# Kernel tuning notes

Measured on AMD Instinct MI355X. Metric: run time of the kernel, lower is better.

## Reference

```python
import jax, jax.numpy as jnp
from jax import lax
import numpy as np

# ---- static config (mirrors init_kwargs) ----
B, IN_CH, OUT_CH, IN_SIZE, OUT_SIZE, W_DIM, K = 8, 512, 512, 64, 64, 512, 3
UP, DOWN, TAPS = 2, 2, 12
IN_CUTOFF = OUT_CUTOFF = 32.0
HALF_W = 32.0 * (np.sqrt(2.0) - 1.0)
TMP_FS = 128.0
CLAMP, SLOPE, ACT_GAIN = 256.0, 0.2, float(np.sqrt(2.0))
HID = 64  # SIREN hidden dim

def _kaiser_beta(a):
    if a > 50:
        return 0.1102 * (a - 8.7)
    if a > 21:
        return 0.5842 * (a - 21.0) ** 0.4 + 0.07886 * (a - 21.0)
    return 0.0

def _firwin(numtaps, cutoff, width, fs):
    # windowed-sinc lowpass (scipy.signal.firwin with kaiser window)
    nyq = fs / 2.0
    atten = 2.285 * (numtaps - 1) * np.pi * (width / nyq) + 7.95
    beta = _kaiser_beta(atten)
    m = np.arange(numtaps) - (numtaps - 1) / 2.0
    c = cutoff / nyq
    h = c * np.sinc(c * m) * np.kaiser(numtaps, beta)
    return (h / h.sum()).astype(np.float32)

UP_FILTER = _firwin(TAPS, IN_CUTOFF, 2 * HALF_W, TMP_FS)
DOWN_FILTER = _firwin(TAPS, OUT_CUTOFF, 2 * HALF_W, TMP_FS)
_pt = (OUT_SIZE - 1) * DOWN + 1 - (IN_SIZE + K - 1) * UP + 2 * TAPS - 2
PAD_LO = (_pt + UP) // 2
PAD_HI = _pt - PAD_LO  # (9, 8)

# ---- SynthesisKernel statics: init_size=3, density=1, down_factor=2, 4-tap filter ----
KG_OUT = 3
KG_IN = KG_OUT * 2  # 6
_kc = KG_OUT / 2.0  # out_cutoff = 1.5
KG_FILT = _firwin(4, _kc, 2 * _kc * (np.sqrt(2.0) - 1.0), _kc * 2 * 2 ** 0.1)
_knots = np.arange(KG_OUT) - KG_OUT // 2
_s2 = (KG_OUT + 2 + 1) / 12.0  # gauss_spline sigma^2 for order out_size+2
_g = np.exp(-_knots ** 2 / (2 * _s2)) / np.sqrt(2 * np.pi * _s2)
GAUSS = (np.sqrt(np.outer(_g, _g)) * 2.0).astype(np.float32)
# affine_grid (align_corners=False) coords scaled by 0.5*in_size/out_size = 1.0
_c = (((2 * np.arange(KG_IN) + 1) / KG_IN) - 1.0) * (0.5 * KG_IN / KG_OUT)
_X, _Y = np.meshgrid(_c, _c)
GRID = np.stack([_X, _Y], -1).reshape(-1, 2).astype(np.float32)  # [36, 2] (x, y)

def _dwconv(x, k):
    return lax.conv_general_dilated(x, k, (1, 1), 'VALID',
        feature_group_count=x.shape[1], dimension_numbers=('NCHW', 'OIHW', 'NCHW'))

def _upfirdn2d(x, f, up=1, down=1, padding=(0, 0, 0, 0), gain=1.0):
    b, c, h, w = x.shape
    if up > 1:
        x = jnp.pad(x[:, :, :, None, :, None], ((0, 0), (0, 0), (0, 0), (0, up - 1), (0, 0), (0, up - 1)))
        x = x.reshape(b, c, h * up, w * up)
    px0, px1, py0, py1 = padding
    x = jnp.pad(x, ((0, 0), (0, 0), (py0, py1), (px0, px1)))
    fl = jnp.flip(f)  # true convolution, like upfirdn2d reference
    x = _dwconv(x, jnp.tile(fl.reshape(1, 1, -1, 1), (c, 1, 1, 1)))
    x = _dwconv(x, jnp.tile(fl.reshape(1, 1, 1, -1), (c, 1, 1, 1)))
    if down > 1:
        x = x[:, :, ::down, ::down]
    return x * gain

def _forward(x, w, affine_w, affine_b, style_weight, bias, siren_w0, siren_b0,
             siren_w1, siren_b1, siren_w2, siren_b2, siren_w3, siren_b3,
             kscale, magnitude_ema):
    # affine: styles [B, IN_CH], weight_gain = 1/sqrt(w_dim), bias_init = 1
    styles = w @ (affine_w.T * (1.0 / np.sqrt(W_DIM))) + affine_b
    # SynthesisKernel: SIREN over 6x6 grid -> filtered/downsampled 3x3 depthwise kernel
    g = jnp.asarray(GRID)
    h1 = jnp.sin(30.0 * (g @ siren_w0 + siren_b0))
    h1 = jnp.sin(h1 @ siren_w1 + siren_b1)
    h1 = jnp.sin(h1 @ siren_w2 + siren_b2)
    kw = h1 @ siren_w3 + siren_b3                                    # [36, IN_CH]
    kw = kw * (jax.nn.sigmoid(kscale / 10.0) * 2.0)
    kw = kw.reshape(1, KG_IN, KG_IN, IN_CH).transpose(3, 0, 1, 2)    # [IN_CH,1,6,6]
    kw = _upfirdn2d(kw, jnp.asarray(KG_FILT), down=2, padding=(1, 1, 1, 1))  # [IN_CH,1,3,3]
    kw = kw - kw.mean(axis=(1, 2, 3), keepdims=True)
    kw = kw * lax.rsqrt(jnp.mean(kw * kw, axis=(1, 2, 3), keepdims=True))
    kw = kw * jnp.asarray(GAUSS)
    # depthwise conv, input_gain = magnitude_ema.rsqrt(), padding = conv_kernel - 1
    kw = kw * lax.rsqrt(magnitude_ema)
    xp = jnp.pad(x, ((0, 0), (0, 0), (K - 1, K - 1), (K - 1, K - 1)))
    x = _dwconv(xp, kw)                                              # [B,IN_CH,66,66]
    # modulated 1x1 conv with demodulation (modulated_conv2d with kh=kw=1)
    sw = style_weight[:, :, 0, 0]                                    # [O, I]
    sw = sw * lax.rsqrt(jnp.mean(sw * sw, axis=1, keepdims=True))
    sn = styles * lax.rsqrt(jnp.mean(styles * styles))
    wb = sw[None, :, :] * sn[:, None, :]                             # [B, O, I]
    wb = wb * lax.rsqrt(jnp.sum(wb * wb, axis=2, keepdims=True) + 1e-8)
    x = jnp.einsum('bihw,boi->bohw', x, wb)
    # filtered leaky relu: bias -> FIR up(2) -> lrelu*sqrt(2), clamp -> FIR down(2)
    x = x + bias[None, :, None, None]
    x = _upfirdn2d(x, jnp.asarray(UP_FILTER), up=UP,
                   padding=(PAD_LO, PAD_HI, PAD_LO, PAD_HI), gain=float(UP * UP))
    x = jnp.where(x < 0, SLOPE * x, x) * ACT_GAIN
    x = jnp.clip(x, -CLAMP, CLAMP)
    x = _upfirdn2d(x, jnp.asarray(DOWN_FILTER), down=DOWN)           # [B,O,64,64]
    return x

def setup_inputs() -> dict:
    key = jax.random.key(0)
    ks = jax.random.split(key, 10)
    ch = float(np.sqrt(6.0 / HID))  # SIREN hidden init bound
    return {
        'x': jax.random.normal(ks[0], (B, IN_CH, IN_SIZE, IN_SIZE), jnp.float32),
        'w': jax.random.normal(ks[1], (B, W_DIM), jnp.float32),
        'affine_w': jax.random.normal(ks[2], (IN_CH, W_DIM), jnp.float32),
        'affine_b': jnp.ones((IN_CH,), jnp.float32),
        'style_weight': jax.random.normal(ks[3], (OUT_CH, IN_CH, 1, 1), jnp.float32),
        'bias': jnp.zeros((OUT_CH,), jnp.float32),
        'siren_w0': jax.random.uniform(ks[4], (2, HID), jnp.float32, -0.5, 0.5),
        'siren_b0': jnp.zeros((HID,), jnp.float32),
        'siren_w1': jax.random.uniform(ks[5], (HID, HID), jnp.float32, -ch, ch),
        'siren_b1': jnp.zeros((HID,), jnp.float32),
        'siren_w2': jax.random.uniform(ks[6], (HID, HID), jnp.float32, -ch, ch),
        'siren_b2': jnp.zeros((HID,), jnp.float32),
        'siren_w3': jax.random.uniform(ks[7], (HID, IN_CH), jnp.float32, -ch, ch),
        'siren_b3': jnp.zeros((IN_CH,), jnp.float32),
        'kscale': jax.random.normal(ks[8], (IN_CH,), jnp.float32),
        'magnitude_ema': jnp.ones((), jnp.float32),
    }

def reference(x, w, affine_w, affine_b, style_weight, bias, siren_w0, siren_b0,
              siren_w1, siren_b1, siren_w2, siren_b2, siren_w3, siren_b3,
              kscale, magnitude_ema):
    return _forward(x, w, affine_w, affine_b, style_weight, bias, siren_w0, siren_b0,
                    siren_w1, siren_b1, siren_w2, siren_b2, siren_w3, siren_b3,
                    kscale, magnitude_ema)
```

## Files before the change

kernel.cpp:

```cpp
#include <hip/hip_runtime.h>
#include <stdint.h>
#include <math.h>

typedef uint16_t u16; typedef uint32_t u32;
typedef __bf16 bf16x8 __attribute__((ext_vector_type(8)));
typedef float  f32x4  __attribute__((ext_vector_type(4)));
typedef u32 __attribute__((address_space(1))) gu32;
typedef u32 __attribute__((address_space(3))) lu32;

#define FOFF_FUP    0
#define FOFF_KG     16
#define FOFF_GAUSS  24
#define FOFF_PART   40
#define FOFF_H3     48
#define FOFF_STYLES 2368
#define FOFF_KK     6464
#define OFFB_WB  ((size_t)65536)
#define OFFB_MUV ((size_t)4456448)
#define OFFB_MUH ((size_t)4459520)
#define OFFB_MDV ((size_t)4487168)
#define OFFB_MDH ((size_t)4489216)
#define OFFB_XT  ((size_t)(8u<<20))
#define OFFB_Y1  ((size_t)(45u<<20))

static __device__ __forceinline__ u16 f2b(float f) {
  union { float f; u32 u; } v; v.f = f;
  u32 u = v.u;
  return (u16)((u + 0x7fffu + ((u >> 16) & 1u)) >> 16);
}
static __device__ __forceinline__ float b2f(u16 h) {
  union { u32 u; float f; } v; v.u = ((u32)h) << 16; return v.f;
}

static __device__ float bessel_i0f(float x) {
  float t = x * 0.5f, t2 = t * t;
  float term = 1.f, sum = 1.f;
  for (int k = 1; k < 32; k++) {
    term *= t2 / ((float)k * (float)k);
    sum += term;
    if (term < 1e-8f * sum) break;
  }
  return sum;
}
static __device__ void firwin_devf(int numtaps, float cutoff, float width, float fs, float* out) {
  float nyq = fs * 0.5f;
  float atten = 2.285f * (numtaps - 1) * 3.14159265358979f * (width / nyq) + 7.95f;
  float beta;
  if (atten > 50.f) beta = 0.1102f * (atten - 8.7f);
  else if (atten > 21.f) beta = 0.5842f * powf(atten - 21.f, 0.4f) + 0.07886f * (atten - 21.f);
  else beta = 0.f;
  float c = cutoff / nyq;
  float i0b = bessel_i0f(beta);
  float h[16]; float s = 0.f;
  for (int n = 0; n < numtaps; n++) {
    float m = n - (numtaps - 1) * 0.5f;
    float x = c * m;
    float pix = 3.14159265358979f * x;
    float snc = (x == 0.f) ? 1.f : __sinf(pix) / pix;
    float r = 2.f * n / (float)(numtaps - 1) - 1.f;
    float arg = 1.f - r * r; if (arg < 0.f) arg = 0.f;
    float kais = bessel_i0f(beta * sqrtf(arg)) / i0b;
    h[n] = c * snc * kais; s += h[n];
  }
  for (int n = 0; n < numtaps; n++) out[n] = h[n] / s;
}

__global__ void k_setup(const float* __restrict__ sw0, const float* __restrict__ sb0,
                        const float* __restrict__ sw1, const float* __restrict__ sb1,
                        const float* __restrict__ sw2, const float* __restrict__ sb2,
                        float* __restrict__ ws) {
  __shared__ float hA[2304], hB[2304];
  int t = threadIdx.x;
  if (t == 0) {
    firwin_devf(12, 32.f, 2.f * 32.f * 0.41421356237309515f, 128.f, ws + FOFF_FUP);
  }
  if (t == 64) {
    float kc = 1.5f;
    firwin_devf(4, kc, 2.f * kc * 0.41421356237309515f, kc * 2.f * 1.0717734625362931f, ws + FOFF_KG);
  }
  if (t == 128) {
    float s2 = 0.5f;
    float gk[3];
    for (int k = 0; k < 3; k++) {
      float kn = (float)(k - 1);
      gk[k] = expf(-kn * kn / (2.f * s2)) / sqrtf(2.f * 3.14159265358979f * s2);
    }
    for (int i = 0; i < 3; i++)
      for (int j = 0; j < 3; j++)
        ws[FOFF_GAUSS + i * 3 + j] = sqrtf(gk[i] * gk[j]) * 2.f;
  }
  if (t >= 192 && t < 200) ws[FOFF_PART + t - 192] = 0.f;
  for (int idx = t; idx < 2304; idx += 256) {
    int p = idx >> 6, u = idx & 63;
    float gx = (2.f * (p % 6) + 1.f) / 6.f - 1.f;
    float gy = (2.f * (p / 6) + 1.f) / 6.f - 1.f;
    hA[idx] = sinf(30.f * (gx * sw0[u] + gy * sw0[64 + u] + sb0[u]));
  }
  __syncthreads();
  {
    float fuv[12];
    #pragma unroll
    for (int i = 0; i < 12; i++) fuv[i] = ws[FOFF_FUP + i];
    char* wsb = (char*)ws;
    u16* muv = (u16*)(wsb + OFFB_MUV);
    u16* muh = (u16*)(wsb + OFFB_MUH);
    u16* mdv = (u16*)(wsb + OFFB_MDV);
    u16* mdh = (u16*)(wsb + OFFB_MDH);
    for (int i = t; i < 48 * 32; i += 256) {
      int r = i >> 5, s = i & 31;
      float v = 0.f;
      if (r < 42 && s < 26) {
        int d = (r >> 1) + 5 - s;
        if (d >= 0 && d <= 5) v = fuv[2 * d + (r & 1)];
      }
      muv[i] = f2b(v);
    }
    for (int i = t; i < 144 * 96; i += 256) {
      int n = i / 96, j = i - n * 96;
      float v = 0.f;
      if (n < 138 && j < 66) {
        int k = (n >> 1) + 1 - j;
        if (k >= 0 && k <= 5) v = fuv[2 * k + (n & 1)];
      }
      muh[i] = f2b(v);
    }
    for (int i = t; i < 16 * 64; i += 256) {
      int R = i >> 6, ar = i & 63;
      float v = 0.f;
      if (ar < 42) {
        int q = ar - 2 * R;
        if (q >= 0 && q <= 11) v = fuv[11 - q];
      }
      mdv[i] = f2b(v);
    }
    for (int i = t; i < 64 * 160; i += 256) {
      int ox = i / 160, ac = i - ox * 160;
      float v = 0.f;
      if (ac < 138) {
        int q = ac - 2 * ox;
        if (q >= 0 && q <= 11) v = fuv[11 - q];
      }
      mdh[i] = f2b(v);
    }
  }
  for (int idx = t; idx < 2304; idx += 256) {
    int p = idx >> 6, u = idx & 63;
    float acc = sb1[u];
    for (int v = 0; v < 64; v++) acc += hA[p * 64 + v] * sw1[v * 64 + u];
    hB[idx] = sinf(acc);
  }
  __syncthreads();
  for (int idx = t; idx < 2304; idx += 256) {
    int p = idx >> 6, u = idx & 63;
    float acc = sb2[u];
    for (int v = 0; v < 64; v++) acc += hB[p * 64 + v] * sw2[v * 64 + u];
    ws[FOFF_H3 + idx] = sinf(acc);
  }
}

__global__ void k_stkw(const float* __restrict__ w, const float* __restrict__ aw,
                       const float* __restrict__ ab,
                       const float* __restrict__ w3, const float* __restrict__ b3,
                       const float* __restrict__ kscale, const float* __restrict__ emap,
                       float* __restrict__ ws) {
  __shared__ __align__(16) char sm[18944];
  int t = threadIdx.x;
  if (blockIdx.x < 64) {
    float* wl  = (float*)sm;
    float* red = (float*)(sm + 2048);
    int b = blockIdx.x >> 3, j0 = (blockIdx.x & 7) * 64;
    wl[t] = w[b * 512 + t]; wl[t + 256] = w[b * 512 + 256 + t];
    __syncthreads();
    int j = j0 + (t & 63), kq = t >> 6;
    const f32x4* ar = (const f32x4*)(aw + (size_t)j * 512 + kq * 128);
    const f32x4* wv = (const f32x4*)(wl + kq * 128);
    float acc = 0.f;
    for (int k = 0; k < 32; k++) {
      f32x4 a = ar[k], c = wv[k];
      acc += a[0] * c[0] + a[1] * c[1] + a[2] * c[2] + a[3] * c[3];
    }
    red[t] = acc; __syncthreads();
    if (t < 64) {
      float sv = (red[t] + red[t + 64] + red[t + 128] + red[t + 192]) * 0.04419417382415922f + ab[j0 + t];
      ws[FOFF_STYLES + b * 512 + j0 + t] = sv;
      float p = sv * sv;
      for (int m = 32; m; m >>= 1) p += __shfl_xor(p, m);
      if (t == 0) atomicAdd(&ws[FOFF_PART + b], p);
    }
  } else {
    float* h3l = (float*)sm;
    float (*kw6)[37] = (float(*)[37])(sm + 9216);
    int c0 = (blockIdx.x - 64) * 64;
    for (int i = t; i < 2304; i += 256) h3l[i] = ws[FOFF_H3 + i];
    __syncthreads();
    int cl = t & 63, pg = t >> 6;
    int c = c0 + cl;
    float acc[9];
    #pragma unroll
    for (int q = 0; q < 9; q++) acc[q] = b3[c];
    for (int v = 0; v < 64; v++) {
      float wv = w3[v * 512 + c];
      #pragma unroll
      for (int q = 0; q < 9; q++) acc[q] += h3l[(pg * 9 + q) * 64 + v] * wv;
    }
    float sc = 2.f / (1.f + expf(-kscale[c] * 0.1f));
    #pragma unroll
    for (int q = 0; q < 9; q++) kw6[cl][pg * 9 + q] = acc[q] * sc;
    __syncthreads();
    if (t < 64) {
      float kg[4];
      #pragma unroll
      for (int i = 0; i < 4; i++) kg[i] = ws[FOFF_KG + i];
      float pre[9];
      for (int u = 0; u < 3; u++)
        for (int vv = 0; vv < 3; vv++) {
          float s = 0.f;
          for (int t1 = 0; t1 < 4; t1++) {
            int a = 2 * u + t1 - 1;
            if (a < 0 || a > 5) continue;
            for (int t2 = 0; t2 < 4; t2++) {
              int bb = 2 * vv + t2 - 1;
              if (bb < 0 || bb > 5) continue;
              s += kg[3 - t1] * kg[3 - t2] * kw6[t][a * 6 + bb];
            }
          }
          pre[u * 3 + vv] = s;
        }
      float m = 0.f;
      #pragma unroll
      for (int q = 0; q < 9; q++) m += pre[q];
      m *= (1.f / 9.f);
      float ms = 0.f;
      #pragma unroll
      for (int q = 0; q < 9; q++) { pre[q] -= m; ms += pre[q] * pre[q]; }
      ms *= (1.f / 9.f);
      float r = 1.f / sqrtf(ms);
      float re = 1.f / sqrtf(emap[0]);
      #pragma unroll
      for (int q = 0; q < 9; q++)
        ws[FOFF_KK + q * 512 + (c0 + t)] = pre[q] * r * ws[FOFF_GAUSS + q] * re;
    }
  }
}

__global__ void k_wb(const float* __restrict__ sw, const float* __restrict__ ws,
                     u16* __restrict__ wb) {
  int wv = threadIdx.x >> 6, lane = threadIdx.x & 63;
  int o = blockIdx.x * 4 + wv, b = blockIdx.y;
  float ssum = 0.f;
  #pragma unroll
  for (int i = 0; i < 8; i++) ssum += ws[FOFF_PART + i];
  float rsn = 1.f / sqrtf(ssum * (1.f / 4096.f));
  float swv[8], stv[8];
  float s2 = 0.f;
  #pragma unroll
  for (int q = 0; q < 8; q++) {
    int i = lane + q * 64;
    swv[q] = sw[(size_t)o * 512 + i];
    stv[q] = ws[FOFF_STYLES + b * 512 + i];
    s2 += swv[q] * swv[q];
  }
  for (int m = 32; m; m >>= 1) s2 += __shfl_xor(s2, m);
  float r1 = 1.f / sqrtf(s2 * (1.f / 512.f));
  float tv[8]; float t2 = 0.f;
  #pragma unroll
  for (int q = 0; q < 8; q++) { tv[q] = swv[q] * r1 * stv[q] * rsn; t2 += tv[q] * tv[q]; }
  for (int m = 32; m; m >>= 1) t2 += __shfl_xor(t2, m);
  float r2 = 1.f / sqrtf(t2 + 1e-8f);
  #pragma unroll
  for (int q = 0; q < 8; q++)
    wb[((size_t)b * 512 + o) * 512 + lane + q * 64] = f2b(tv[q] * r2);
}

__global__ void k_transpose(const float* __restrict__ x, u16* __restrict__ xT) {
  int h = blockIdx.x, c0 = blockIdx.y * 64, b = blockIdx.z;
  int t = threadIdx.x;
  __shared__ u16 tl[64][66];
  int wcol = t & 63, cbase = t >> 6;
  const float* xp = x + ((size_t)(b * 512 + c0)) * 4096 + h * 64;
  #pragma unroll
  for (int k = 0; k < 16; k++) {
    int ci = cbase + k * 4;
    tl[ci][wcol] = f2b(xp[(size_t)ci * 4096 + wcol]);
  }
  __syncthreads();
  int cp = t & 31, wbse = t >> 5;
  u32* dst = (u32*)(xT + ((size_t)b * 4096 + h * 64) * 512 + c0);
  #pragma unroll
  for (int k = 0; k < 8; k++) {
    int w_ = wbse + k * 8;
    u32 v0 = tl[cp * 2][w_], v1 = tl[cp * 2 + 1][w_];
    dst[w_ * 256 + cp] = v0 | (v1 << 16);
  }
}

__global__ void k_dw(const u16* __restrict__ xT, const float* __restrict__ ws,
                     u16* __restrict__ y1) {
  int tile = blockIdx.x, b = blockIdx.y, t = threadIdx.x;
  int c2 = t * 2;
  float2 kk[9];
  #pragma unroll
  for (int q = 0; q < 9; q++) kk[q] = *(const float2*)&ws[FOFF_KK + q * 512 + c2];
  #pragma unroll 2
  for (int pos = 0; pos < 16; pos++) {
    int hw = tile * 16 + pos;
    if (hw < 4356) {
      int h = hw / 66, w_ = hw - h * 66;
      float a0 = 0.f, a1 = 0.f;
      for (int i = 0; i < 3; i++) {
        int ih = h - 2 + i; if (ih < 0 || ih >= 64) continue;
        for (int j = 0; j < 3; j++) {
          int iw = w_ - 2 + j; if (iw < 0 || iw >= 64) continue;
          u32 xv = *(const u32*)(xT + ((size_t)b * 4096 + ih * 64 + iw) * 512 + c2);
          float2 kv = kk[i * 3 + j];
          a0 += kv.x * b2f((u16)xv);
          a1 += kv.y * b2f((u16)(xv >> 16));
        }
      }
      ((u32*)y1)[(((size_t)b * 4480 + hw) * 512 + c2) >> 1] = (u32)f2b(a0) | ((u32)f2b(a1) << 16);
    } else {
      ((u32*)y1)[(((size_t)b * 4480 + hw) * 512 + c2) >> 1] = 0u;
    }
  }
}

__launch_bounds__(256, 4)
__global__ void k_gemm(const u16* __restrict__ wbm, const u16* __restrict__ y1,
                       const float* __restrict__ bias, u16* __restrict__ y2) {
  int lid = blockIdx.x + 35 * (blockIdx.y + (blockIdx.z << 2));
  int b  = lid & 7;
  int s_ = lid >> 3;
  int mt = s_ & 3;
  int nt = s_ >> 2;
  int t = threadIdx.x, lane = t & 63, wv = t >> 6;
  int wm = wv >> 1, wn = wv & 1;
  __shared__ u16 Al[4096];
  __shared__ u16 Bl[4096];
  f32x4 acc[4][4];
  #pragma unroll
  for (int i = 0; i < 4; i++)
    #pragma unroll
    for (int j = 0; j < 4; j++)
      acc[i][j] = (f32x4){0.f, 0.f, 0.f, 0.f};

  const size_t Abase = (size_t)b * 512 + mt * 128;
  const size_t Bbase = (size_t)b * 4480 + nt * 128;
  int lrow = lane >> 2, dch = lane & 3;
  int cp = lane >> 4;

  for (int ks = 0; ks < 16; ks++) {
    int k0 = ks * 32;
    __syncthreads();
    #pragma unroll
    for (int half = 0; half < 2; half++) {
      int rbase = half * 64 + wv * 16;
      int row = rbase + lrow;
      int gch = dch ^ ((row >> 1) & 3);
      const u16* ga = wbm + (Abase + row) * 512 + k0 + gch * 8;
      const u16* gb = y1 + (Bbase + row) * 512 + k0 + gch * 8;
      __builtin_amdgcn_global_load_lds((const gu32*)ga, (lu32*)&Al[rbase * 32], 16, 0, 0);
      __builtin_amdgcn_global_load_lds((const gu32*)gb, (lu32*)&Bl[rbase * 32], 16, 0, 0);
    }
    asm volatile("s_waitcnt vmcnt(0)" ::: "memory");
    __syncthreads();
    bf16x8 af[4], bfr[4];
    #pragma unroll
    for (int mi = 0; mi < 4; mi++) {
      int row = wm * 64 + mi * 16 + (lane & 15);
      af[mi] = *(const bf16x8*)&Al[row * 32 + ((cp ^ ((row >> 1) & 3)) * 8)];
    }
    #pragma unroll
    for (int ni = 0; ni < 4; ni++) {
      int row = wn * 64 + ni * 16 + (lane & 15);
      bfr[ni] = *(const bf16x8*)&Bl[row * 32 + ((cp ^ ((row >> 1) & 3)) * 8)];
    }
    #pragma unroll
    for (int mi = 0; mi < 4; mi++)
      #pragma unroll
      for (int ni = 0; ni < 4; ni++)
        acc[mi][ni] = __builtin_amdgcn_mfma_f32_16x16x32_bf16(af[mi], bfr[ni], acc[mi][ni], 0, 0, 0);
  }
  int col0 = nt * 128 + wn * 64 + (lane & 15);
  int rb = (lane >> 4) * 4;
  #pragma unroll
  for (int mi = 0; mi < 4; mi++) {
    #pragma unroll
    for (int j = 0; j < 4; j++) {
      int o = mt * 128 + wm * 64 + mi * 16 + rb + j;
      float bv = bias[o];
      size_t rowoff = ((size_t)b * 512 + o) * 4480;
      #pragma unroll
      for (int ni = 0; ni < 4; ni++)
        y2[rowoff + col0 + ni * 16] = f2b(acc[mi][ni][j] + bv);
    }
  }
}

__launch_bounds__(256, 5)
__global__ void k_updown(const u16* __restrict__ y2,
                         const u16* __restrict__ muv, const u16* __restrict__ muh,
                         const u16* __restrict__ mdv, const u16* __restrict__ mdh,
                         float* __restrict__ out) {
  int g = blockIdx.x, o = blockIdx.y, b = blockIdx.z;
  int t = threadIdx.x, lane = t & 63, wv = t >> 6;
  int l15 = lane & 15, cp = lane >> 4, rb = cp * 4;
  __shared__ __align__(16) char smem[30720];
  u16* Yt  = (u16*)smem;
  u16* At  = (u16*)smem;
  u16* T1u = (u16*)(smem + 20736);
  u16* T3u = (u16*)(smem + 20736);
  const int out_r0 = g * 16;
  const int yrow0 = out_r0 - 4;
  const u16* plane = y2 + ((size_t)b * 512 + o) * 4480;

  for (int i = t; i < 1920; i += 256) ((float4*)smem)[i] = make_float4(0.f, 0.f, 0.f, 0.f);
  __syncthreads();
  for (int idx = t; idx < 26 * 66; idx += 256) {
    int s = idx / 66, j = idx - 66 * s;
    int grow = yrow0 + s;
    u16 v = 0;
    if (grow >= 0 && grow < 66) v = plane[(size_t)grow * 66 + j];
    Yt[j * 40 + s] = v;
  }
  __syncthreads();

  __builtin_amdgcn_s_setprio(1);
  for (int tau = wv; tau < 15; tau += 4) {
    int mi = tau / 5, ni = tau - mi * 5;
    bf16x8 a = *(const bf16x8*)&muv[(mi * 16 + l15) * 32 + cp * 8];
    bf16x8 bfr = *(const bf16x8*)&Yt[(ni * 16 + l15) * 40 + cp * 8];
    f32x4 acc = (f32x4){0.f, 0.f, 0.f, 0.f};
    acc = __builtin_amdgcn_mfma_f32_16x16x32_bf16(a, bfr, acc, 0, 0, 0);
    #pragma unroll
    for (int j = 0; j < 4; j++)
      T1u[(mi * 16 + rb + j) * 104 + ni * 16 + l15] = f2b(acc[j]);
  }
  __builtin_amdgcn_s_setprio(0);
  __syncthreads();

  __builtin_amdgcn_s_setprio(1);
  for (int ni = wv; ni < 9; ni += 4) {
    bf16x8 bh[3];
    #pragma unroll
    for (int ks = 0; ks < 3; ks++)
      bh[ks] = *(const bf16x8*)&muh[(ni * 16 + l15) * 96 + ks * 32 + cp * 8];
    #pragma unroll
    for (int mi = 0; mi < 3; mi++) {
      f32x4 acc = (f32x4){0.f, 0.f, 0.f, 0.f};
      #pragma unroll
      for (int ks = 0; ks < 3; ks++) {
        bf16x8 a = *(const bf16x8*)&T1u[(mi * 16 + l15) * 104 + ks * 32 + cp * 8];
        acc = __builtin_amdgcn_mfma_f32_16x16x32_bf16(a, bh[ks], acc, 0, 0, 0);
      }
      int c = ni * 16 + l15;
      u16 pv[4];
      #pragma unroll
      for (int j = 0; j < 4; j++) {
        float x = acc[j];
        x = fmaxf(x, 0.2f * x) * 5.65685424949238f;
        x = fminf(fmaxf(x, -256.f), 256.f);
        pv[j] = f2b(x);
      }
      u32 lo = (u32)pv[0] | ((u32)pv[1] << 16);
      u32 hi = (u32)pv[2] | ((u32)pv[3] << 16);
      *(uint2*)&At[c * 72 + mi * 16 + rb] = make_uint2(lo, hi);
    }
  }
  __builtin_amdgcn_s_setprio(0);
  __syncthreads();

  __builtin_amdgcn_s_setprio(1);
  {
    bf16x8 a0 = *(const bf16x8*)&mdv[l15 * 64 + cp * 8];
    bf16x8 a1 = *(const bf16x8*)&mdv[l15 * 64 + 32 + cp * 8];
    for (int ni = wv; ni < 9; ni += 4) {
      f32x4 acc = (f32x4){0.f, 0.f, 0.f, 0.f};
      bf16x8 b0 = *(const bf16x8*)&At[(ni * 16 + l15) * 72 + cp * 8];
      acc = __builtin_amdgcn_mfma_f32_16x16x32_bf16(a0, b0, acc, 0, 0, 0);
      bf16x8 b1 = *(const bf16x8*)&At[(ni * 16 + l15) * 72 + 32 + cp * 8];
      acc = __builtin_amdgcn_mfma_f32_16x16x32_bf16(a1, b1, acc, 0, 0, 0);
      #pragma unroll
      for (int j = 0; j < 4; j++)
        T3u[(rb + j) * 168 + ni * 16 + l15] = f2b(acc[j]);
    }
  }
  __builtin_amdgcn_s_setprio(0);
  __syncthreads();

  {
    __builtin_amdgcn_s_setprio(1);
    f32x4 acc = (f32x4){0.f, 0.f, 0.f, 0.f};
    #pragma unroll
    for (int ks = 0; ks < 5; ks++) {
      bf16x8 a = *(const bf16x8*)&T3u[l15 * 168 + ks * 32 + cp * 8];
      bf16x8 bfr = *(const bf16x8*)&mdh[(wv * 16 + l15) * 160 + ks * 32 + cp * 8];
      acc = __builtin_amdgcn_mfma_f32_16x16x32_bf16(a, bfr, acc, 0, 0, 0);
    }
    __builtin_amdgcn_s_setprio(0);
    float* op = out + (((size_t)b * 512 + o) * 64 + out_r0) * 64;
    #pragma unroll
    for (int j = 0; j < 4; j++)
      op[(rb + j) * 64 + wv * 16 + l15] = acc[j];
  }
}

extern "C" void kernel_launch(void* const* d_in, const int* in_sizes, int n_in,
                              void* d_out, int out_size, void* d_ws, size_t ws_size,
                              hipStream_t stream) {
  const float* x     = (const float*)d_in[0];
  const float* w     = (const float*)d_in[1];
  const float* aw    = (const float*)d_in[2];
  const float* ab    = (const float*)d_in[3];
  const float* swgt  = (const float*)d_in[4];
  const float* bias  = (const float*)d_in[5];
  const float* sw0   = (const float*)d_in[6];
  const float* sb0   = (const float*)d_in[7];
  const float* sw1   = (const float*)d_in[8];
  const float* sb1   = (const float*)d_in[9];
  const float* sw2   = (const float*)d_in[10];
  const float* sb2   = (const float*)d_in[11];
  const float* sw3   = (const float*)d_in[12];
  const float* sb3   = (const float*)d_in[13];
  const float* kscl  = (const float*)d_in[14];
  const float* ema   = (const float*)d_in[15];

  float* ws  = (float*)d_ws;
  char*  wsb = (char*)d_ws;
  u16* wbp = (u16*)(wsb + OFFB_WB);
  u16* xT  = (u16*)(wsb + OFFB_XT);
  u16* y2  = xT;
  u16* y1  = (u16*)(wsb + OFFB_Y1);
  u16* muv = (u16*)(wsb + OFFB_MUV);
  u16* muh = (u16*)(wsb + OFFB_MUH);
  u16* mdv = (u16*)(wsb + OFFB_MDV);
  u16* mdh = (u16*)(wsb + OFFB_MDH);

  k_setup<<<dim3(1), dim3(256), 0, stream>>>(sw0, sb0, sw1, sb1, sw2, sb2, ws);
  k_stkw<<<dim3(72), dim3(256), 0, stream>>>(w, aw, ab, sw3, sb3, kscl, ema, ws);
  k_wb<<<dim3(128, 8), dim3(256), 0, stream>>>(swgt, ws, wbp);
  k_transpose<<<dim3(64, 8, 8), dim3(256), 0, stream>>>(x, xT);
  k_dw<<<dim3(280, 8), dim3(256), 0, stream>>>(xT, ws, y1);
  k_gemm<<<dim3(35, 4, 8), dim3(256), 0, stream>>>(wbp, y1, bias, y2);
  k_updown<<<dim3(4, 512, 8), dim3(256), 0, stream>>>(y2, muv, muh, mdv, mdh, (float*)d_out);
}
```

Measured before the change: 300.6 us.

## Fuse NCHW-to-NHWC transpose into depthwise conv using LDS row staging

Replaces the separate transpose kernel and the depthwise 3x3 kernel with one kernel. Each block stages three padded input rows for 64 channels in shared memory, converted to bf16, then computes the 66 output columns for one row straight from LDS. This removes the round trip through the intermediate bf16 NHWC buffer and one kernel launch, and reads each input value once per block instead of up to nine times from global memory. In exchange, each input row is loaded by three blocks, the fp32 global loads are strided per channel, and the LDS accesses may bank-conflict.

```diff
diff --git a/kernel.cpp b/kernel.cpp
--- a/kernel.cpp
+++ b/kernel.cpp
@@ -20,7 +20,7 @@
 #define OFFB_MUH ((size_t)4459520)
 #define OFFB_MDV ((size_t)4487168)
 #define OFFB_MDH ((size_t)4489216)
-#define OFFB_XT  ((size_t)(8u<<20))
+#define OFFB_Y2  ((size_t)(8u<<20))
 #define OFFB_Y1  ((size_t)(45u<<20))
 
 static __device__ __forceinline__ u16 f2b(float f) {
@@ -272,55 +272,58 @@
     wb[((size_t)b * 512 + o) * 512 + lane + q * 64] = f2b(tv[q] * r2);
 }
 
-__global__ void k_transpose(const float* __restrict__ x, u16* __restrict__ xT) {
-  int h = blockIdx.x, c0 = blockIdx.y * 64, b = blockIdx.z;
-  int t = threadIdx.x;
-  __shared__ u16 tl[64][66];
-  int wcol = t & 63, cbase = t >> 6;
-  const float* xp = x + ((size_t)(b * 512 + c0)) * 4096 + h * 64;
-  #pragma unroll
-  for (int k = 0; k < 16; k++) {
-    int ci = cbase + k * 4;
-    tl[ci][wcol] = f2b(xp[(size_t)ci * 4096 + wcol]);
-  }
-  __syncthreads();
-  int cp = t & 31, wbse = t >> 5;
-  u32* dst = (u32*)(xT + ((size_t)b * 4096 + h * 64) * 512 + c0);
-  #pragma unroll
-  for (int k = 0; k < 8; k++) {
-    int w_ = wbse + k * 8;
-    u32 v0 = tl[cp * 2][w_], v1 = tl[cp * 2 + 1][w_];
-    dst[w_ * 256 + cp] = v0 | (v1 << 16);
-  }
-}
-
-__global__ void k_dw(const u16* __restrict__ xT, const float* __restrict__ ws,
-                     u16* __restrict__ y1) {
-  int tile = blockIdx.x, b = blockIdx.y, t = threadIdx.x;
-  int c2 = t * 2;
+__global__ void k_tdw(const float* __restrict__ x, const float* __restrict__ ws,
+                      u16* __restrict__ y1) {
+  int h = blockIdx.x, cb = blockIdx.y, b = blockIdx.z;
+  int c0 = cb * 64, t = threadIdx.x;
+  if (h == 66) {
+    u32* dst = (u32*)y1;
+    for (int idx = t; idx < 124 * 32; idx += 256) {
+      int row = idx >> 5, col = idx & 31;
+      dst[((size_t)b * 4480 + 4356 + row) * 256 + (c0 >> 1) + col] = 0u;
+    }
+    return;
+  }
+  __shared__ u16 xl[3 * 68 * 64];
+  for (int idx = t; idx < 3 * 4 * 64; idx += 256) {
+    int i = idx >> 8, r = idx & 255;
+    int wsl = r >> 6; wsl = (wsl < 2) ? wsl : (64 + wsl);
+    xl[i * 4352 + wsl * 64 + (r & 63)] = 0;
+  }
+  for (int slot = t; slot < 768; slot += 256) {
+    int c = slot & 63, ri = slot >> 6;
+    int i = ri >> 2, q = ri & 3;
+    int ih = h - 2 + i;
+    u16* dst = &xl[i * 4352 + (2 + q * 16) * 64 + c];
+    if (ih >= 0 && ih < 64) {
+      const float* xp = x + ((size_t)(b * 512 + c0 + c)) * 4096 + ih * 64 + q * 16;
+      #pragma unroll
+      for (int k = 0; k < 16; k++) dst[k * 64] = f2b(xp[k]);
+    } else {
+      #pragma unroll
+      for (int k = 0; k < 16; k++) dst[k * 64] = 0;
+    }
+  }
+  __syncthreads();
+  int c2i = t & 31, wg = t >> 5;
+  int c2 = 2 * c2i;
   float2 kk[9];
   #pragma unroll
-  for (int q = 0; q < 9; q++) kk[q] = *(const float2*)&ws[FOFF_KK + q * 512 + c2];
-  #pragma unroll 2
-  for (int pos = 0; pos < 16; pos++) {
-    int hw = tile * 16 + pos;
-    if (hw < 4356) {
-      int h = hw / 66, w_ = hw - h * 66;
-      float a0 = 0.f, a1 = 0.f;
-      for (int i = 0; i < 3; i++) {
-        int ih = h - 2 + i; if (ih < 0 || ih >= 64) continue;
-        for (int j = 0; j < 3; j++) {
-          int iw = w_ - 2 + j; if (iw < 0 || iw >= 64) continue;
-          u32 xv = *(const u32*)(xT + ((size_t)b * 4096 + ih * 64 + iw) * 512 + c2);
-          float2 kv = kk[i * 3 + j];
-          a0 += kv.x * b2f((u16)xv);
-          a1 += kv.y * b2f((u16)(xv >> 16));
-        }
-      }
-      ((u32*)y1)[(((size_t)b * 4480 + hw) * 512 + c2) >> 1] = (u32)f2b(a0) | ((u32)f2b(a1) << 16);
-    } else {
-      ((u32*)y1)[(((size_t)b * 4480 + hw) * 512 + c2) >> 1] = 0u;
-    }
+  for (int q = 0; q < 9; q++) kk[q] = *(const float2*)&ws[FOFF_KK + q * 512 + c0 + c2];
+  for (int w_ = wg; w_ < 66; w_ += 8) {
+    float a0 = 0.f, a1 = 0.f;
+    #pragma unroll
+    for (int i = 0; i < 3; i++) {
+      #pragma unroll
+      for (int j = 0; j < 3; j++) {
+        u32 xv = *(const u32*)&xl[i * 4352 + (w_ + j) * 64 + c2];
+        float2 kv = kk[i * 3 + j];
+        a0 += kv.x * b2f((u16)xv);
+        a1 += kv.y * b2f((u16)(xv >> 16));
+      }
+    }
+    ((u32*)y1)[(((size_t)b * 4480 + h * 66 + w_) * 512 + c0 + c2) >> 1] =
+        (u32)f2b(a0) | ((u32)f2b(a1) << 16);
   }
 }
 
@@ -527,8 +530,7 @@
   float* ws  = (float*)d_ws;
   char*  wsb = (char*)d_ws;
   u16* wbp = (u16*)(wsb + OFFB_WB);
-  u16* xT  = (u16*)(wsb + OFFB_XT);
-  u16* y2  = xT;
+  u16* y2  = (u16*)(wsb + OFFB_Y2);
   u16* y1  = (u16*)(wsb + OFFB_Y1);
   u16* muv = (u16*)(wsb + OFFB_MUV);
   u16* muh = (u16*)(wsb + OFFB_MUH);
@@ -538,8 +540,7 @@
   k_setup<<<dim3(1), dim3(256), 0, stream>>>(sw0, sb0, sw1, sb1, sw2, sb2, ws);
   k_stkw<<<dim3(72), dim3(256), 0, stream>>>(w, aw, ab, sw3, sb3, kscl, ema, ws);
   k_wb<<<dim3(128, 8), dim3(256), 0, stream>>>(swgt, ws, wbp);
-  k_transpose<<<dim3(64, 8, 8), dim3(256), 0, stream>>>(x, xT);
-  k_dw<<<dim3(280, 8), dim3(256), 0, stream>>>(xT, ws, y1);
+  k_tdw<<<dim3(67, 8, 8), dim3(256), 0, stream>>>(x, ws, y1);
   k_gemm<<<dim3(35, 4, 8), dim3(256), 0, stream>>>(wbp, y1, bias, y2);
   k_updown<<<dim3(4, 512, 8), dim3(256), 0, stream>>>(y2, muv, muh, mdv, mdh, (float*)d_out);
 }
```

Measured after the change: 253.2 us. 1.19x faster.
